# Optimization experiments

Measured on AMD Instinct MI355X. Metric: run time of the kernel, lower is better.

## Reference

```python
import jax, jax.numpy as jnp
import numpy as np

N = 100000   # total nodes across the ragged graph batch
E = 800000   # edges
B = 4096     # graphs
V = 103      # element vocab (embedding rows)
D_IN = 200   # embedding dim
H = 256      # hidden dim


def setup_inputs() -> dict:
    key = jax.random.key(0)
    ks = jax.random.split(key, 20)
    s = 0.05
    return {
        "weight": jax.random.normal(ks[0], (V, D_IN), jnp.float32),
        "sto_x": jax.random.randint(ks[1], (N,), 0, V),
        "sto_edge_index": jax.random.randint(ks[2], (2, E), 0, N),
        "sto_weight": jax.random.uniform(ks[3], (N,), jnp.float32),
        "sto_batch": jnp.sort(jax.random.randint(ks[4], (N,), 0, B)),
        "gW0": jax.random.normal(ks[5], (D_IN, H), jnp.float32) * s,
        "gb0": jnp.zeros((H,), jnp.float32),
        "gW1": jax.random.normal(ks[6], (H, H), jnp.float32) * s,
        "gb1": jnp.zeros((H,), jnp.float32),
        "gW2": jax.random.normal(ks[7], (H, H), jnp.float32) * s,
        "gb2": jnp.zeros((H,), jnp.float32),
        "lstm_Wih": jax.random.normal(ks[8], (4 * H, 2 * H), jnp.float32) * s,
        "lstm_Whh": jax.random.normal(ks[9], (4 * H, H), jnp.float32) * s,
        "lstm_bih": jnp.zeros((4 * H,), jnp.float32),
        "lstm_bhh": jnp.zeros((4 * H,), jnp.float32),
        "mlin_W": jax.random.normal(ks[10], (H, 2 * H), jnp.float32) * s,
        "mlin_b": jnp.zeros((H,), jnp.float32),
        "p0W": jax.random.normal(ks[11], (128, H), jnp.float32) * s,
        "p0b": jnp.zeros((128,), jnp.float32),
        "p1W": jax.random.normal(ks[12], (128, 128), jnp.float32) * s,
        "p1b": jnp.zeros((128,), jnp.float32),
        "p2W": jax.random.normal(ks[13], (1, 128), jnp.float32) * s,
        "p2b": jnp.zeros((1,), jnp.float32),
    }


def reference(weight, sto_x, sto_edge_index, sto_weight, sto_batch,
              gW0, gb0, gW1, gb1, gW2, gb2,
              lstm_Wih, lstm_Whh, lstm_bih, lstm_bhh,
              mlin_W, mlin_b, p0W, p0b, p1W, p1b, p2W, p2b):
    # embedding gather (sto_x - 1, with -1 wrapping to the last row as in torch)
    x = weight[sto_x - 1]

    # --- GCN (3 layers, symmetric norm with self-loops, ReLU between layers) ---
    loop = jnp.arange(N)
    src = jnp.concatenate([sto_edge_index[0], loop])
    dst = jnp.concatenate([sto_edge_index[1], loop])
    deg = jax.ops.segment_sum(jnp.ones_like(dst, jnp.float32), dst, N)
    dinv = jax.lax.rsqrt(jnp.maximum(deg, 1.0))
    norm = (dinv[src] * dinv[dst])[:, None]

    def conv(h_in, W, b):
        hw = h_in @ W                                   # [N, H]
        return jax.ops.segment_sum(hw[src] * norm, dst, N) + b

    x = jax.nn.relu(conv(x, gW0, gb0))
    x = jax.nn.relu(conv(x, gW1, gb1))
    x = conv(x, gW2, gb2)

    # --- stoichiometric weighting + graph-wise scatter sum ---
    wx = x * sto_weight[:, None]                        # [N, H]
    sto = jax.ops.segment_sum(wx, sto_batch, B)         # [B, H]

    # --- Set2Set pooling (2 processing steps, 1-layer LSTM) ---
    h = jnp.zeros((B, H), wx.dtype)
    c = jnp.zeros((B, H), wx.dtype)
    q_star = jnp.zeros((B, 2 * H), wx.dtype)
    for _ in range(2):
        gates = q_star @ lstm_Wih.T + lstm_bih + h @ lstm_Whh.T + lstm_bhh
        i, f, g, o = jnp.split(gates, 4, axis=-1)
        c = jax.nn.sigmoid(f) * c + jax.nn.sigmoid(i) * jnp.tanh(g)
        h = jax.nn.sigmoid(o) * jnp.tanh(c)
        e = jnp.sum(wx * h[sto_batch], axis=-1)         # [N]
        emax = jax.ops.segment_max(e, sto_batch, B)
        a = jnp.exp(e - emax[sto_batch])
        a = a / (jax.ops.segment_sum(a, sto_batch, B)[sto_batch] + 1e-16)
        r = jax.ops.segment_sum(wx * a[:, None], sto_batch, B)
        q_star = jnp.concatenate([h, r], axis=-1)

    mean = q_star @ mlin_W.T + mlin_b + sto
    mean = mean / jnp.maximum(jnp.linalg.norm(mean, axis=1, keepdims=True), 1e-12)

    # --- predictor MLP (LeakyReLU slope 0.01) ---
    y = jax.nn.leaky_relu(mean @ p0W.T + p0b)
    y = jax.nn.leaky_relu(y @ p1W.T + p1b)
    return y @ p2W.T + p2b                              # [B, 1]
```

## Files before the change

### kernel.cpp

```cpp
#include <hip/hip_runtime.h>
#include <math.h>

constexpr int Nn  = 100000;
constexpr int Ee  = 800000;
constexpr int Bb  = 4096;
constexpr int Vv  = 103;
constexpr int DIN = 200;
constexpr int Hh  = 256;

constexpr int SCHUNK = 1024;
constexpr int NSCAN  = (Nn + SCHUNK - 1)/SCHUNK;

using short8 = __attribute__((ext_vector_type(8))) short;
using f32x4  = __attribute__((ext_vector_type(4))) float;

__device__ __forceinline__ float sigf(float x){ return 1.f/(1.f+expf(-x)); }

__device__ __forceinline__ unsigned short f2bf(float f){
  unsigned int u = __float_as_uint(f);
  u += 0x7FFFu + ((u >> 16) & 1u);
  return (unsigned short)(u >> 16);
}
__device__ __forceinline__ float bf2f(unsigned int u){
  return __uint_as_float((u & 0xFFFFu) << 16);
}

constexpr int PW_A = DIN*Hh;
constexpr int PW_B = Hh*Hh;
constexpr int PW_C = Hh*Hh;
constexpr int PW_D = 4*Hh*3*Hh;
constexpr int PW_E = Hh*2*Hh;
constexpr int PW_F = 128*Hh;
constexpr int PW_G = 128*128;
constexpr int PW_H = Bb + 1;
constexpr int PW_I = 4*Hh;
constexpr int PW_TOT = PW_A+PW_B+PW_C+PW_D+PW_E+PW_F+PW_G+PW_H+PW_I;

__global__ void k_prep(const float* __restrict__ gW0, float* __restrict__ gW0t,
                       const float* __restrict__ gW1, unsigned short* __restrict__ gW1tb,
                       const float* __restrict__ gW2, unsigned short* __restrict__ gW2tb,
                       const float* __restrict__ Wih, const float* __restrict__ Whh,
                       unsigned short* __restrict__ Wpb,
                       const float* __restrict__ mW, unsigned short* __restrict__ mWb,
                       const float* __restrict__ p0W, unsigned short* __restrict__ p0Wb,
                       const float* __restrict__ p1W, unsigned short* __restrict__ p1Wb,
                       const int* __restrict__ batch, int* __restrict__ boffs,
                       const float* __restrict__ bih, const float* __restrict__ bhh,
                       float* __restrict__ bsum){
  int idx = blockIdx.x*256 + threadIdx.x;
  if (idx >= PW_TOT) return;
  if (idx < PW_A){
    int r = idx / Hh, c = idx % Hh;
    gW0t[(size_t)c*DIN + r] = gW0[idx];
    return;
  }
  idx -= PW_A;
  if (idx < PW_B){
    int r = idx >> 8, c = idx & 255;
    gW1tb[(size_t)c*Hh + r] = f2bf(gW1[idx]);
    return;
  }
  idx -= PW_B;
  if (idx < PW_C){
    int r = idx >> 8, c = idx & 255;
    gW2tb[(size_t)c*Hh + r] = f2bf(gW2[idx]);
    return;
  }
  idx -= PW_C;
  if (idx < PW_D){
    int g = idx / (3*Hh), j = idx % (3*Hh);
    float v = (j < 2*Hh) ? Wih[(size_t)g*2*Hh + j] : Whh[(size_t)g*Hh + (j - 2*Hh)];
    Wpb[idx] = f2bf(v);
    return;
  }
  idx -= PW_D;
  if (idx < PW_E){ mWb[idx] = f2bf(mW[idx]); return; }
  idx -= PW_E;
  if (idx < PW_F){ p0Wb[idx] = f2bf(p0W[idx]); return; }
  idx -= PW_F;
  if (idx < PW_G){ p1Wb[idx] = f2bf(p1W[idx]); return; }
  idx -= PW_G;
  if (idx < PW_H){
    int b = idx;
    int lo = 0, hi = Nn;
    while (lo < hi){ int mid = (lo+hi)>>1; if (batch[mid] < b) lo = mid+1; else hi = mid; }
    boffs[b] = lo;
    return;
  }
  idx -= PW_H;
  bsum[idx] = bih[idx] + bhh[idx];
}

__global__ void k_count(const int* __restrict__ dst, int* __restrict__ counts){
  int e = blockIdx.x*256 + threadIdx.x;
  if (e < Ee) atomicAdd(&counts[dst[e]], 1);
}

__global__ void k_scan1(const int* __restrict__ counts, int* __restrict__ partial,
                        float* __restrict__ dinv){
  __shared__ int red[256];
  int t = threadIdx.x;
  int base = blockIdx.x*SCHUNK + t*4;
  int s = 0;
  if (base + 3 < Nn){
    int4 v = *reinterpret_cast<const int4*>(counts + base);
    s = v.x+v.y+v.z+v.w;
    dinv[base]   = rsqrtf((float)(v.x + 1));
    dinv[base+1] = rsqrtf((float)(v.y + 1));
    dinv[base+2] = rsqrtf((float)(v.z + 1));
    dinv[base+3] = rsqrtf((float)(v.w + 1));
  } else {
    for (int i=0;i<4;++i) if (base+i<Nn){ int c = counts[base+i]; s += c; dinv[base+i] = rsqrtf((float)(c+1)); }
  }
  red[t] = s; __syncthreads();
  for (int st=128; st>0; st>>=1){ if (t<st) red[t]+=red[t+st]; __syncthreads(); }
  if (t==0) partial[blockIdx.x] = red[0];
}

__global__ void k_scan2(int* __restrict__ partial, int n){
  __shared__ int buf[128];
  int t = threadIdx.x;
  int v = (t < n) ? partial[t] : 0;
  buf[t] = v; __syncthreads();
  for (int off=1; off<128; off<<=1){
    int tv = (t>=off) ? buf[t-off] : 0;
    __syncthreads();
    buf[t] += tv;
    __syncthreads();
  }
  if (t < n) partial[t] = buf[t] - v;
}

__global__ void k_scan3(const int* __restrict__ counts, const int* __restrict__ partial,
                        int* __restrict__ offs, int* __restrict__ fptr){
  __shared__ int red[256];
  int t = threadIdx.x;
  int base = blockIdx.x*SCHUNK + t*4;
  int c0=0,c1=0,c2=0,c3=0;
  if (base + 3 < Nn){ int4 v = *reinterpret_cast<const int4*>(counts + base); c0=v.x;c1=v.y;c2=v.z;c3=v.w; }
  else { if (base<Nn) c0=counts[base]; if (base+1<Nn) c1=counts[base+1];
         if (base+2<Nn) c2=counts[base+2]; if (base+3<Nn) c3=counts[base+3]; }
  int s = c0+c1+c2+c3;
  red[t] = s; __syncthreads();
  for (int off=1; off<256; off<<=1){
    int tv = (t>=off) ? red[t-off] : 0;
    __syncthreads();
    red[t] += tv;
    __syncthreads();
  }
  int run = partial[blockIdx.x] + red[t] - s;
  if (base   < Nn){ offs[base]   = run; fptr[base]   = run; } run += c0;
  if (base+1 < Nn){ offs[base+1] = run; fptr[base+1] = run; } run += c1;
  if (base+2 < Nn){ offs[base+2] = run; fptr[base+2] = run; } run += c2;
  if (base+3 < Nn){ offs[base+3] = run; fptr[base+3] = run; } run += c3;
  if (blockIdx.x == gridDim.x-1 && t == 255) offs[Nn] = partial[blockIdx.x] + red[255];
}

__global__ void k_fill(const int* __restrict__ ei, const float* __restrict__ dinv,
                       const int* __restrict__ sto_x, int* __restrict__ fptr,
                       uint2* __restrict__ epack, unsigned char* __restrict__ evoc){
  int e = blockIdx.x*256 + threadIdx.x;
  if (e >= Ee) return;
  int s = ei[e], d = ei[Ee + e];
  int pos = atomicAdd(&fptr[d], 1);
  epack[pos] = make_uint2((unsigned int)s, __float_as_uint(dinv[s]*dinv[d]));
  int v = sto_x[s];
  evoc[pos] = (unsigned char)((v == 0) ? (Vv-1) : v-1);
}

__global__ void k_conv0(const unsigned short* __restrict__ WG0b, const int* __restrict__ sto_x,
                        const int* __restrict__ offs, const uint2* __restrict__ epack,
                        const unsigned char* __restrict__ evoc, const float* __restrict__ dinv,
                        const float* __restrict__ bias, unsigned short* __restrict__ Xb){
  int wid = threadIdx.x >> 6, lane = threadIdx.x & 63;
  int n = blockIdx.x*4 + wid;
  const uint2* Wv = (const uint2*)WG0b;
  int v0 = sto_x[n]; int r0 = (v0 == 0) ? (Vv-1) : v0-1;
  float dn = dinv[n]; float s2 = dn*dn;
  uint2 w0 = Wv[(size_t)r0*64 + lane];
  float a0 = bf2f(w0.x)*s2, a1 = bf2f(w0.x>>16)*s2;
  float a2 = bf2f(w0.y)*s2, a3 = bf2f(w0.y>>16)*s2;
  int s = offs[n], e = offs[n+1];
  int k = s;
  for (; k + 7 < e; k += 8){
    uint2 ev[8]; int rv[8]; uint2 g[8];
    #pragma unroll
    for (int j = 0; j < 8; ++j){ ev[j] = epack[k+j]; rv[j] = evoc[k+j]; }
    #pragma unroll
    for (int j = 0; j < 8; ++j) g[j] = Wv[(size_t)rv[j]*64 + lane];
    #pragma unroll
    for (int j = 0; j < 8; ++j){
      float nn = __uint_as_float(ev[j].y);
      a0 += bf2f(g[j].x)*nn; a1 += bf2f(g[j].x>>16)*nn;
      a2 += bf2f(g[j].y)*nn; a3 += bf2f(g[j].y>>16)*nn;
    }
  }
  for (; k < e; ++k){
    uint2 ev = epack[k];
    uint2 g = Wv[(size_t)evoc[k]*64 + lane];
    float nn = __uint_as_float(ev.y);
    a0 += bf2f(g.x)*nn; a1 += bf2f(g.x>>16)*nn;
    a2 += bf2f(g.y)*nn; a3 += bf2f(g.y>>16)*nn;
  }
  float4 bv = ((const float4*)bias)[lane];
  a0 = fmaxf(a0 + bv.x, 0.f); a1 = fmaxf(a1 + bv.y, 0.f);
  a2 = fmaxf(a2 + bv.z, 0.f); a3 = fmaxf(a3 + bv.w, 0.f);
  uint2 o;
  o.x = (unsigned int)f2bf(a0) | ((unsigned int)f2bf(a1) << 16);
  o.y = (unsigned int)f2bf(a2) | ((unsigned int)f2bf(a3) << 16);
  ((uint2*)Xb)[(size_t)n*64 + lane] = o;
}

__global__ void k_agg(const unsigned short* __restrict__ Xb, const int* __restrict__ offs,
                      const uint2* __restrict__ epack, const float* __restrict__ dinv,
                      unsigned short* __restrict__ T){
  int wid = threadIdx.x >> 6, lane = threadIdx.x & 63;
  int n = blockIdx.x*4 + wid;
  const uint2* Xv = (const uint2*)Xb;
  uint2 v = Xv[(size_t)n*64 + lane];
  float dn = dinv[n]; float s2 = dn*dn;
  float a0 = bf2f(v.x)*s2, a1 = bf2f(v.x>>16)*s2;
  float a2 = bf2f(v.y)*s2, a3 = bf2f(v.y>>16)*s2;
  int s = offs[n], e = offs[n+1];
  int k = s;
  for (; k + 7 < e; k += 8){
    uint2 ev[8], g[8];
    #pragma unroll
    for (int j = 0; j < 8; ++j) ev[j] = epack[k+j];
    #pragma unroll
    for (int j = 0; j < 8; ++j) g[j] = Xv[(size_t)ev[j].x*64 + lane];
    #pragma unroll
    for (int j = 0; j < 8; ++j){
      float nn = __uint_as_float(ev[j].y);
      a0 += bf2f(g[j].x)*nn; a1 += bf2f(g[j].x>>16)*nn;
      a2 += bf2f(g[j].y)*nn; a3 += bf2f(g[j].y>>16)*nn;
    }
  }
  for (; k + 1 < e; k += 2){
    uint2 e0 = epack[k], e1 = epack[k+1];
    uint2 g0 = Xv[(size_t)e0.x*64 + lane];
    uint2 g1 = Xv[(size_t)e1.x*64 + lane];
    float n0 = __uint_as_float(e0.y), n1 = __uint_as_float(e1.y);
    a0 += bf2f(g0.x)*n0; a1 += bf2f(g0.x>>16)*n0; a2 += bf2f(g0.y)*n0; a3 += bf2f(g0.y>>16)*n0;
    a0 += bf2f(g1.x)*n1; a1 += bf2f(g1.x>>16)*n1; a2 += bf2f(g1.y)*n1; a3 += bf2f(g1.y>>16)*n1;
  }
  if (k < e){
    uint2 e0 = epack[k];
    uint2 g0 = Xv[(size_t)e0.x*64 + lane];
    float n0 = __uint_as_float(e0.y);
    a0 += bf2f(g0.x)*n0; a1 += bf2f(g0.x>>16)*n0;
    a2 += bf2f(g0.y)*n0; a3 += bf2f(g0.y>>16)*n0;
  }
  uint2 o;
  o.x = (unsigned int)f2bf(a0) | ((unsigned int)f2bf(a1) << 16);
  o.y = (unsigned int)f2bf(a2) | ((unsigned int)f2bf(a3) << 16);
  ((uint2*)T)[(size_t)n*64 + lane] = o;
}

__global__ __launch_bounds__(512) void k_gemm64(
    const unsigned short* __restrict__ A, int lda,
    const unsigned short* __restrict__ Bt,
    const float* __restrict__ bias, const float* __restrict__ rowscale,
    const float* __restrict__ addf,
    float* __restrict__ Cf, unsigned short* __restrict__ Cb,
    int M, int K, int Nc, int relu)
{
  __shared__ unsigned short lds[23040];
  unsigned short (*Al)[72] = (unsigned short(*)[72])lds;
  unsigned short (*Bl)[72] = (unsigned short(*)[72])(lds + 64*72);

  int tid = threadIdx.x;
  int w = tid >> 6, lane = tid & 63;
  int wr = (w >> 2)*32, wc = (w & 3)*64;
  int l16 = lane & 15, kh = lane >> 4;
  int rbase = blockIdx.y*64, cbase = blockIdx.x*256;
  int sr = tid >> 3, sb = tid & 7;

  f32x4 acc[2][4] = {};

  for (int k0 = 0; k0 < K; k0 += 64){
    int kk = k0 + sb*8;
    uint4 a0 = make_uint4(0,0,0,0);
    int ar = rbase + sr;
    if (ar < M) a0 = *reinterpret_cast<const uint4*>(A + (size_t)ar*lda + kk);
    uint4 b0 = *reinterpret_cast<const uint4*>(Bt + (size_t)(cbase + sr      )*K + kk);
    uint4 b1 = *reinterpret_cast<const uint4*>(Bt + (size_t)(cbase + sr +  64)*K + kk);
    uint4 b2 = *reinterpret_cast<const uint4*>(Bt + (size_t)(cbase + sr + 128)*K + kk);
    uint4 b3 = *reinterpret_cast<const uint4*>(Bt + (size_t)(cbase + sr + 192)*K + kk);
    __syncthreads();
    *reinterpret_cast<uint4*>(&Al[sr][sb*8])     = a0;
    *reinterpret_cast<uint4*>(&Bl[sr][sb*8])     = b0;
    *reinterpret_cast<uint4*>(&Bl[sr+64][sb*8])  = b1;
    *reinterpret_cast<uint4*>(&Bl[sr+128][sb*8]) = b2;
    *reinterpret_cast<uint4*>(&Bl[sr+192][sb*8]) = b3;
    __syncthreads();

    #pragma unroll
    for (int kq = 0; kq < 2; ++kq){
      short8 af[2], bfv[4];
      #pragma unroll
      for (int m = 0; m < 2; ++m)
        af[m] = *reinterpret_cast<const short8*>(&Al[wr + m*16 + l16][kq*32 + kh*8]);
      #pragma unroll
      for (int n2 = 0; n2 < 4; ++n2)
        bfv[n2] = *reinterpret_cast<const short8*>(&Bl[wc + n2*16 + l16][kq*32 + kh*8]);
      #pragma unroll
      for (int m = 0; m < 2; ++m)
        #pragma unroll
        for (int n2 = 0; n2 < 4; ++n2)
          acc[m][n2] = __builtin_amdgcn_mfma_f32_16x16x32_bf16(af[m], bfv[n2], acc[m][n2], 0, 0, 0);
    }
  }

  if (Cf){
    #pragma unroll
    for (int n2 = 0; n2 < 4; ++n2){
      int col = cbase + wc + n2*16 + l16;
      float bv = bias ? bias[col] : 0.f;
      #pragma unroll
      for (int m = 0; m < 2; ++m){
        #pragma unroll
        for (int i = 0; i < 4; ++i){
          int row = rbase + wr + m*16 + kh*4 + i;
          if (row >= M) continue;
          float v = acc[m][n2][i] + bv;
          if (addf) v += addf[(size_t)row*Nc + col];
          if (rowscale) v *= rowscale[row];
          if (relu == 1) v = fmaxf(v, 0.f);
          else if (relu == 2) v = (v > 0.f) ? v : 0.01f*v;
          Cf[(size_t)row*Nc + col] = v;
        }
      }
    }
  }
  if (Cb){
    __syncthreads();
    unsigned short* eps = lds + w*(32*72);
    #pragma unroll
    for (int n2 = 0; n2 < 4; ++n2){
      int colg = cbase + wc + n2*16 + l16;
      float bv = bias ? bias[colg] : 0.f;
      #pragma unroll
      for (int m = 0; m < 2; ++m){
        #pragma unroll
        for (int i = 0; i < 4; ++i){
          int lrow = m*16 + kh*4 + i;
          int rowg = rbase + wr + lrow;
          float v = acc[m][n2][i] + bv;
          float rs = (rowscale && rowg < M) ? rowscale[rowg] : 1.f;
          v *= rs;
          if (relu == 1) v = fmaxf(v, 0.f);
          else if (relu == 2) v = (v > 0.f) ? v : 0.01f*v;
          eps[lrow*72 + n2*16 + l16] = f2bf(v);
        }
      }
    }
    int c8 = lane & 7;
    #pragma unroll
    for (int rd = 0; rd < 4; ++rd){
      int lrow = rd*8 + (lane >> 3);
      int rowg = rbase + wr + lrow;
      short8 vv = *reinterpret_cast<const short8*>(&eps[lrow*72 + c8*8]);
      if (rowg < M)
        *reinterpret_cast<short8*>(Cb + (size_t)rowg*Nc + cbase + wc + c8*8) = vv;
    }
  }
}

__global__ __launch_bounds__(512) void k_gemm8(
    const unsigned short* __restrict__ A, int lda,
    const unsigned short* __restrict__ Bt,
    const float* __restrict__ bias, const float* __restrict__ rowscale,
    const float* __restrict__ addf,
    float* __restrict__ Cf, unsigned short* __restrict__ Cb,
    int M, int K, int Nc, int relu)
{
  __shared__ unsigned short lds[18432];
  unsigned short (*Al)[40] = (unsigned short(*)[40])lds;
  unsigned short (*Bl)[40] = (unsigned short(*)[40])(lds + 128*40);

  int tid = threadIdx.x;
  int w = tid >> 6, lane = tid & 63;
  int wr = (w >> 1)*32, wc = (w & 1)*64;
  int l16 = lane & 15, kh = lane >> 4;
  int rbase = blockIdx.y*128, cbase = blockIdx.x*128;
  int sr = tid >> 2, sb = tid & 3;

  f32x4 acc[2][4] = {};

  for (int k0 = 0; k0 < K; k0 += 32){
    int kk = k0 + sb*8;
    uint4 a0 = make_uint4(0,0,0,0);
    int ar0 = rbase + sr;
    if (ar0 < M) a0 = *reinterpret_cast<const uint4*>(A + (size_t)ar0*lda + kk);
    uint4 b0 = *reinterpret_cast<const uint4*>(Bt + (size_t)(cbase + sr)*K + kk);
    __syncthreads();
    *reinterpret_cast<uint4*>(&Al[sr][sb*8]) = a0;
    *reinterpret_cast<uint4*>(&Bl[sr][sb*8]) = b0;
    __syncthreads();

    short8 af[2], bfv[4];
    #pragma unroll
    for (int m = 0; m < 2; ++m) af[m] = *reinterpret_cast<const short8*>(&Al[wr + m*16 + l16][kh*8]);
    #pragma unroll
    for (int n2 = 0; n2 < 4; ++n2) bfv[n2] = *reinterpret_cast<const short8*>(&Bl[wc + n2*16 + l16][kh*8]);
    #pragma unroll
    for (int m = 0; m < 2; ++m)
      #pragma unroll
      for (int n2 = 0; n2 < 4; ++n2)
        acc[m][n2] = __builtin_amdgcn_mfma_f32_16x16x32_bf16(af[m], bfv[n2], acc[m][n2], 0, 0, 0);
  }

  if (Cf){
    #pragma unroll
    for (int n2 = 0; n2 < 4; ++n2){
      int col = cbase + wc + n2*16 + l16;
      float bv = bias ? bias[col] : 0.f;
      #pragma unroll
      for (int m = 0; m < 2; ++m){
        #pragma unroll
        for (int i = 0; i < 4; ++i){
          int row = rbase + wr + m*16 + kh*4 + i;
          if (row >= M) continue;
          float v = acc[m][n2][i] + bv;
          if (addf) v += addf[(size_t)row*Nc + col];
          if (rowscale) v *= rowscale[row];
          if (relu == 1) v = fmaxf(v, 0.f);
          else if (relu == 2) v = (v > 0.f) ? v : 0.01f*v;
          Cf[(size_t)row*Nc + col] = v;
        }
      }
    }
  }
  if (Cb){
    __syncthreads();
    unsigned short* eps = lds + w*(32*72);
    #pragma unroll
    for (int n2 = 0; n2 < 4; ++n2){
      int colg = cbase + wc + n2*16 + l16;
      float bv = bias ? bias[colg] : 0.f;
      #pragma unroll
      for (int m = 0; m < 2; ++m){
        #pragma unroll
        for (int i = 0; i < 4; ++i){
          int lrow = m*16 + kh*4 + i;
          int rowg = rbase + wr + lrow;
          float v = acc[m][n2][i] + bv;
          float rs = (rowscale && rowg < M) ? rowscale[rowg] : 1.f;
          v *= rs;
          if (relu == 1) v = fmaxf(v, 0.f);
          else if (relu == 2) v = (v > 0.f) ? v : 0.01f*v;
          eps[lrow*72 + n2*16 + l16] = f2bf(v);
        }
      }
    }
    int c8 = lane & 7;
    #pragma unroll
    for (int rd = 0; rd < 4; ++rd){
      int lrow = rd*8 + (lane >> 3);
      int rowg = rbase + wr + lrow;
      short8 vv = *reinterpret_cast<const short8*>(&eps[lrow*72 + c8*8]);
      if (rowg < M)
        *reinterpret_cast<short8*>(Cb + (size_t)rowg*Nc + cbase + wc + c8*8) = vv;
    }
  }
}

__global__ __launch_bounds__(256) void k_gemm_nt(
    const float* __restrict__ A, const float* __restrict__ Bt,
    float* __restrict__ C, unsigned short* __restrict__ Cb,
    int M, int K, int Nc)
{
  __shared__ float As[64][20];
  __shared__ float Bs[64][20];
  int tid = threadIdx.x;
  int rbase = blockIdx.y*64, cbase = blockIdx.x*64;
  int ty = tid>>4, tx = tid&15;
  int lr = tid>>2, lq = tid&3;
  float acc[4][4] = {};
  for (int k0 = 0; k0 < K; k0 += 16){
    float4 av = make_float4(0,0,0,0), bv = make_float4(0,0,0,0);
    int kk = k0 + lq*4;
    int ar = rbase + lr;
    if (ar < M && kk < K){
      if (kk + 3 < K) av = *reinterpret_cast<const float4*>(A + (size_t)ar*K + kk);
      else { float t0[4] = {0,0,0,0}; for (int i=0; i<4 && kk+i<K; ++i) t0[i] = A[(size_t)ar*K + kk + i];
             av = make_float4(t0[0],t0[1],t0[2],t0[3]); }
    }
    int br = cbase + lr;
    if (br < Nc && kk < K){
      if (kk + 3 < K) bv = *reinterpret_cast<const float4*>(Bt + (size_t)br*K + kk);
      else { float t0[4] = {0,0,0,0}; for (int i=0; i<4 && kk+i<K; ++i) t0[i] = Bt[(size_t)br*K + kk + i];
             bv = make_float4(t0[0],t0[1],t0[2],t0[3]); }
    }
    __syncthreads();
    *reinterpret_cast<float4*>(&As[lr][lq*4]) = av;
    *reinterpret_cast<float4*>(&Bs[lr][lq*4]) = bv;
    __syncthreads();
    #pragma unroll
    for (int kc = 0; kc < 16; kc += 4){
      float4 a4[4], b4[4];
      #pragma unroll
      for (int i=0;i<4;++i) a4[i] = *reinterpret_cast<float4*>(&As[ty*4+i][kc]);
      #pragma unroll
      for (int j=0;j<4;++j) b4[j] = *reinterpret_cast<float4*>(&Bs[tx*4+j][kc]);
      #pragma unroll
      for (int i=0;i<4;++i)
        #pragma unroll
        for (int j=0;j<4;++j)
          acc[i][j] += a4[i].x*b4[j].x + a4[i].y*b4[j].y + a4[i].z*b4[j].z + a4[i].w*b4[j].w;
    }
  }
  #pragma unroll
  for (int i=0;i<4;++i){
    int r = rbase + ty*4 + i;
    if (r >= M) continue;
    #pragma unroll
    for (int j=0;j<4;++j){
      int cc = cbase + tx*4 + j;
      if (cc >= Nc) continue;
      float v = acc[i][j];
      if (C)  C[(size_t)r*Nc + cc] = v;
      if (Cb) Cb[(size_t)r*Nc + cc] = f2bf(v);
    }
  }
}

__global__ void k_lstm(const float* __restrict__ gates, float* __restrict__ cbuf,
                       float* __restrict__ hbuf, unsigned short* __restrict__ qh){
  int idx = blockIdx.x*256 + threadIdx.x;
  if (idx >= Bb*Hh) return;
  int b = idx >> 8, ch = idx & 255;
  const float* g = gates + (size_t)b*4*Hh;
  float ig = sigf(g[ch]);
  float fg = sigf(g[Hh + ch]);
  float gg = tanhf(g[2*Hh + ch]);
  float og = sigf(g[3*Hh + ch]);
  float cn = fg*cbuf[idx] + ig*gg;
  float hn = og*tanhf(cn);
  cbuf[idx] = cn; hbuf[idx] = hn;
  unsigned short hb = f2bf(hn);
  qh[(size_t)b*3*Hh + ch] = hb;
  qh[(size_t)b*3*Hh + 2*Hh + ch] = hb;
}

__global__ void k_pool(const unsigned short* __restrict__ wxb,
                       const float* __restrict__ hbuf,
                       const int* __restrict__ boffs,
                       unsigned short* __restrict__ qh,
                       float* __restrict__ sto, int do_sto){
  int wid = threadIdx.x >> 6, lane = threadIdx.x & 63;
  int g = blockIdx.x*4 + wid;
  if (g >= Bb) return;
  const uint2* Xv = (const uint2*)wxb;
  float4 hv = ((const float4*)hbuf)[(size_t)g*64 + lane];
  int s = boffs[g], e = boffs[g+1];
  float m = -INFINITY, ssum = 0.f;
  float a0=0.f,a1=0.f,a2=0.f,a3=0.f;
  float t0=0.f,t1=0.f,t2=0.f,t3=0.f;
  for (int n = s; n < e; ++n){
    uint2 v = Xv[(size_t)n*64 + lane];
    float x0=bf2f(v.x), x1=bf2f(v.x>>16), x2=bf2f(v.y), x3=bf2f(v.y>>16);
    if (do_sto){ t0+=x0; t1+=x1; t2+=x2; t3+=x3; }
    float d = x0*hv.x + x1*hv.y + x2*hv.z + x3*hv.w;
    #pragma unroll
    for (int mask=32; mask; mask>>=1) d += __shfl_xor(d, mask, 64);
    if (d > m){
      float sc = expf(m - d);
      ssum = ssum*sc + 1.f;
      a0 = a0*sc + x0; a1 = a1*sc + x1; a2 = a2*sc + x2; a3 = a3*sc + x3;
      m = d;
    } else {
      float p = expf(d - m);
      ssum += p;
      a0 += p*x0; a1 += p*x1; a2 += p*x2; a3 += p*x3;
    }
  }
  float inv = 1.f/(ssum + 1e-16f);
  uint2 o;
  o.x = (unsigned int)f2bf(a0*inv) | ((unsigned int)f2bf(a1*inv) << 16);
  o.y = (unsigned int)f2bf(a2*inv) | ((unsigned int)f2bf(a3*inv) << 16);
  ((uint2*)(qh + (size_t)g*3*Hh + Hh))[lane] = o;
  if (do_sto) ((float4*)sto)[(size_t)g*64 + lane] = make_float4(t0,t1,t2,t3);
}

__global__ void k_norm(float* __restrict__ mean, unsigned short* __restrict__ outb){
  __shared__ float red[256];
  int b = blockIdx.x, tid = threadIdx.x;
  float v = mean[(size_t)b*Hh + tid];
  red[tid] = v*v; __syncthreads();
  for (int st=128; st>0; st>>=1){ if (tid<st) red[tid] += red[tid+st]; __syncthreads(); }
  float nrm = fmaxf(sqrtf(red[0]), 1e-12f);
  float o = v/nrm;
  outb[(size_t)b*Hh + tid] = f2bf(o);
}

__global__ void k_out(const float* __restrict__ y1, const float* __restrict__ p2W,
                      const float* __restrict__ p2b, float* __restrict__ out){
  __shared__ float red[128];
  int b = blockIdx.x, tid = threadIdx.x;
  float v = y1[(size_t)b*128 + tid]*p2W[tid];
  red[tid] = v; __syncthreads();
  for (int st=64; st>0; st>>=1){ if (tid<st) red[tid] += red[tid+st]; __syncthreads(); }
  if (tid == 0) out[b] = red[0] + p2b[0];
}

extern "C" void kernel_launch(void* const* d_in, const int* in_sizes, int n_in,
                              void* d_out, int out_size, void* d_ws, size_t ws_size,
                              hipStream_t stream) {
  const float* weight   = (const float*)d_in[0];
  const int*   sto_x    = (const int*)  d_in[1];
  const int*   ei       = (const int*)  d_in[2];
  const float* sto_w    = (const float*)d_in[3];
  const int*   batch    = (const int*)  d_in[4];
  const float* gW0 = (const float*)d_in[5];   const float* gb0 = (const float*)d_in[6];
  const float* gW1 = (const float*)d_in[7];   const float* gb1 = (const float*)d_in[8];
  const float* gW2 = (const float*)d_in[9];   const float* gb2 = (const float*)d_in[10];
  const float* Wih = (const float*)d_in[11];  const float* Whh = (const float*)d_in[12];
  const float* bih = (const float*)d_in[13];  const float* bhh = (const float*)d_in[14];
  const float* mW  = (const float*)d_in[15];  const float* mb  = (const float*)d_in[16];
  const float* p0W = (const float*)d_in[17];  const float* p0b = (const float*)d_in[18];
  const float* p1W = (const float*)d_in[19];  const float* p1b = (const float*)d_in[20];
  const float* p2W = (const float*)d_in[21];  const float* p2b = (const float*)d_in[22];
  float* out = (float*)d_out;

  char* w = (char*)d_ws;
  auto alloc = [&](size_t bytes)->char*{ char* p = w; w += (bytes + 255) & ~size_t(255); return p; };
  unsigned short* Xb = (unsigned short*)alloc((size_t)Nn*Hh*2);
  unsigned short* Tb = (unsigned short*)alloc((size_t)Nn*Hh*2);
  float* WG0   = (float*)alloc((size_t)Vv*Hh*4);
  unsigned short* WG0b = (unsigned short*)alloc((size_t)Vv*Hh*2);
  float* gW0t  = (float*)alloc((size_t)Hh*DIN*4);
  unsigned short* gW1tb = (unsigned short*)alloc((size_t)Hh*Hh*2);
  unsigned short* gW2tb = (unsigned short*)alloc((size_t)Hh*Hh*2);
  unsigned short* Wpb   = (unsigned short*)alloc((size_t)4*Hh*3*Hh*2);
  unsigned short* mWb   = (unsigned short*)alloc((size_t)Hh*2*Hh*2);
  unsigned short* p0Wb  = (unsigned short*)alloc((size_t)128*Hh*2);
  unsigned short* p1Wb  = (unsigned short*)alloc((size_t)128*128*2);
  int*   counts= (int*)  alloc((size_t)Nn*4);
  int*   offs  = (int*)  alloc((size_t)(Nn+1)*4);
  int*   fptr  = (int*)  alloc((size_t)Nn*4);
  int*   spart = (int*)  alloc((size_t)NSCAN*4);
  float* dinv  = (float*)alloc((size_t)Nn*4);
  uint2* epack = (uint2*)alloc((size_t)Ee*8);
  unsigned char* evoc = (unsigned char*)alloc((size_t)Ee);
  int*   boffs = (int*)  alloc((size_t)(Bb+1)*4);
  float* sto   = (float*)alloc((size_t)Bb*Hh*4);
  float* hbuf  = (float*)alloc((size_t)Bb*Hh*4);
  float* cbuf  = (float*)alloc((size_t)Bb*Hh*4);
  unsigned short* qh = (unsigned short*)alloc((size_t)Bb*3*Hh*2);
  float* gates = (float*)alloc((size_t)Bb*4*Hh*4);
  float* bsum  = (float*)alloc((size_t)4*Hh*4);
  float* meanb = (float*)alloc((size_t)Bb*Hh*4);
  unsigned short* meanbb = (unsigned short*)alloc((size_t)Bb*Hh*2);
  unsigned short* y0b = (unsigned short*)alloc((size_t)Bb*128*2);
  float* y1    = (float*)alloc((size_t)Bb*128*4);

  auto gemm8 = [&](const unsigned short* A, int lda, const unsigned short* Bt,
                   const float* bias, const float* rowscale, const float* addf,
                   float* Cf, unsigned short* Cb, int M, int K, int Nc, int relu){
    dim3 g(Nc/128, (M+127)/128);
    k_gemm8<<<g, 512, 0, stream>>>(A, lda, Bt, bias, rowscale, addf, Cf, Cb, M, K, Nc, relu);
  };
  auto gemm64 = [&](const unsigned short* A, int lda, const unsigned short* Bt,
                    const float* bias, const float* rowscale, const float* addf,
                    float* Cf, unsigned short* Cb, int M, int K, int Nc, int relu){
    dim3 g(Nc/256, (M+63)/64);
    k_gemm64<<<g, 512, 0, stream>>>(A, lda, Bt, bias, rowscale, addf, Cf, Cb, M, K, Nc, relu);
  };

  hipMemsetAsync(counts, 0, (size_t)Nn*4, stream);
  hipMemsetAsync(cbuf,  0, (size_t)Bb*Hh*4, stream);
  hipMemsetAsync(qh,    0, (size_t)Bb*3*Hh*2, stream);

  k_prep<<<(PW_TOT+255)/256, 256, 0, stream>>>(
      gW0, gW0t, gW1, gW1tb, gW2, gW2tb, Wih, Whh, Wpb,
      mW, mWb, p0W, p0Wb, p1W, p1Wb, batch, boffs, bih, bhh, bsum);

  k_count<<<(Ee+255)/256, 256, 0, stream>>>(ei + Ee, counts);
  k_scan1<<<NSCAN, 256, 0, stream>>>(counts, spart, dinv);
  k_scan2<<<1, 128, 0, stream>>>(spart, NSCAN);
  k_scan3<<<NSCAN, 256, 0, stream>>>(counts, spart, offs, fptr);
  k_fill<<<(Ee+255)/256, 256, 0, stream>>>(ei, dinv, sto_x, fptr, epack, evoc);

  {
    dim3 g((Hh+63)/64, (Vv+63)/64);
    k_gemm_nt<<<g, 256, 0, stream>>>(weight, gW0t, WG0, WG0b, Vv, DIN, Hh);
  }
  k_conv0<<<Nn/4, 256, 0, stream>>>(WG0b, sto_x, offs, epack, evoc, dinv, gb0, Xb);

  k_agg<<<Nn/4, 256, 0, stream>>>(Xb, offs, epack, dinv, Tb);
  gemm64(Tb, Hh, gW1tb, gb1, nullptr, nullptr, nullptr, Xb, Nn, Hh, Hh, 1);
  k_agg<<<Nn/4, 256, 0, stream>>>(Xb, offs, epack, dinv, Tb);
  gemm64(Tb, Hh, gW2tb, gb2, sto_w, nullptr, nullptr, Xb, Nn, Hh, Hh, 0);

  for (int t = 0; t < 2; ++t){
    gemm64(qh, 3*Hh, Wpb, bsum, nullptr, nullptr, gates, nullptr, Bb, 3*Hh, 4*Hh, 0);
    k_lstm<<<(Bb*Hh+255)/256, 256, 0, stream>>>(gates, cbuf, hbuf, qh);
    k_pool<<<Bb/4, 256, 0, stream>>>(Xb, hbuf, boffs, qh, sto, t == 0);
  }

  gemm64(qh, 3*Hh, mWb, mb, nullptr, sto, meanb, nullptr, Bb, 2*Hh, Hh, 0);
  k_norm<<<Bb, Hh, 0, stream>>>(meanb, meanbb);
  gemm8(meanbb, Hh, p0Wb, p0b, nullptr, nullptr, nullptr, y0b, Bb, Hh, 128, 2);
  gemm8(y0b, 128, p1Wb, p1b, nullptr, nullptr, y1, nullptr, Bb, 128, 128, 2);
  k_out<<<Bb, 128, 0, stream>>>(y1, p2W, p2b, out);
}
```

Baseline: 551.0 us.

## Fold constant first Set2Set LSTM step and shrink second-step gate GEMM

Because h, c and q_star start at zero, the first LSTM step gives the same h0/c0 for every graph, so it is computed once by a tiny kernel instead of a full gate GEMM over all graphs. The second step's gate contribution from h0 (Wih's h-part plus Whh) is folded into a per-gate constant bias, leaving a GEMM with K=256 over only the attention readout r. The pool kernel is also unrolled by two nodes to overlap loads and shuffle reductions, and the memsets for the zeroed LSTM state and the unused fp32 embedding output are dropped. In exchange it adds small extra kernels, and it relies on the initial state being zero, which the reference specifies.

```diff
diff --git a/kernel.cpp b/kernel.cpp
--- a/kernel.cpp
+++ b/kernel.cpp
@@ -28,7 +28,7 @@
 constexpr int PW_A = DIN*Hh;
 constexpr int PW_B = Hh*Hh;
 constexpr int PW_C = Hh*Hh;
-constexpr int PW_D = 4*Hh*3*Hh;
+constexpr int PW_D = 4*Hh*Hh;
 constexpr int PW_E = Hh*2*Hh;
 constexpr int PW_F = 128*Hh;
 constexpr int PW_G = 128*128;
@@ -39,8 +39,7 @@
 __global__ void k_prep(const float* __restrict__ gW0, float* __restrict__ gW0t,
                        const float* __restrict__ gW1, unsigned short* __restrict__ gW1tb,
                        const float* __restrict__ gW2, unsigned short* __restrict__ gW2tb,
-                       const float* __restrict__ Wih, const float* __restrict__ Whh,
-                       unsigned short* __restrict__ Wpb,
+                       const float* __restrict__ Wih, unsigned short* __restrict__ WihRb,
                        const float* __restrict__ mW, unsigned short* __restrict__ mWb,
                        const float* __restrict__ p0W, unsigned short* __restrict__ p0Wb,
                        const float* __restrict__ p1W, unsigned short* __restrict__ p1Wb,
@@ -68,9 +67,8 @@
   }
   idx -= PW_C;
   if (idx < PW_D){
-    int g = idx / (3*Hh), j = idx % (3*Hh);
-    float v = (j < 2*Hh) ? Wih[(size_t)g*2*Hh + j] : Whh[(size_t)g*Hh + (j - 2*Hh)];
-    Wpb[idx] = f2bf(v);
+    int gi = idx >> 8, k = idx & 255;
+    WihRb[idx] = f2bf(Wih[(size_t)gi*2*Hh + Hh + k]);
     return;
   }
   idx -= PW_D;
@@ -89,6 +87,30 @@
   }
   idx -= PW_H;
   bsum[idx] = bih[idx] + bhh[idx];
+}
+
+__global__ void k_h0(const float* __restrict__ bsum, float* __restrict__ h0,
+                     float* __restrict__ c0){
+  int ch = threadIdx.x;
+  float ig = sigf(bsum[ch]);
+  float gg = tanhf(bsum[2*Hh + ch]);
+  float og = sigf(bsum[3*Hh + ch]);
+  float cn = ig*gg;
+  float hn = og*tanhf(cn);
+  c0[ch] = cn; h0[ch] = hn;
+}
+
+__global__ void k_gconst(const float* __restrict__ Wih, const float* __restrict__ Whh,
+                         const float* __restrict__ bsum, const float* __restrict__ h0,
+                         float* __restrict__ gconst){
+  int wid = threadIdx.x >> 6, lane = threadIdx.x & 63;
+  int gi = blockIdx.x*4 + wid;
+  float4 hv = ((const float4*)h0)[lane];
+  float4 a = *reinterpret_cast<const float4*>(Wih + (size_t)gi*2*Hh + lane*4);
+  float4 b = *reinterpret_cast<const float4*>(Whh + (size_t)gi*Hh  + lane*4);
+  float ssum = hv.x*(a.x+b.x) + hv.y*(a.y+b.y) + hv.z*(a.z+b.z) + hv.w*(a.w+b.w);
+  for (int off=32; off; off>>=1) ssum += __shfl_down(ssum, off, 64);
+  if (lane == 0) gconst[gi] = bsum[gi] + ssum;
 }
 
 __global__ void k_count(const int* __restrict__ dst, int* __restrict__ counts){
@@ -468,8 +490,7 @@
 
 __global__ __launch_bounds__(256) void k_gemm_nt(
     const float* __restrict__ A, const float* __restrict__ Bt,
-    float* __restrict__ C, unsigned short* __restrict__ Cb,
-    int M, int K, int Nc)
+    unsigned short* __restrict__ Cb, int M, int K, int Nc)
 {
   __shared__ float As[64][20];
   __shared__ float Bs[64][20];
@@ -519,15 +540,13 @@
     for (int j=0;j<4;++j){
       int cc = cbase + tx*4 + j;
       if (cc >= Nc) continue;
-      float v = acc[i][j];
-      if (C)  C[(size_t)r*Nc + cc] = v;
-      if (Cb) Cb[(size_t)r*Nc + cc] = f2bf(v);
-    }
-  }
-}
-
-__global__ void k_lstm(const float* __restrict__ gates, float* __restrict__ cbuf,
-                       float* __restrict__ hbuf, unsigned short* __restrict__ qh){
+      Cb[(size_t)r*Nc + cc] = f2bf(acc[i][j]);
+    }
+  }
+}
+
+__global__ void k_lstm1(const float* __restrict__ gates, const float* __restrict__ c0,
+                        float* __restrict__ hbuf, unsigned short* __restrict__ qh2){
   int idx = blockIdx.x*256 + threadIdx.x;
   if (idx >= Bb*Hh) return;
   int b = idx >> 8, ch = idx & 255;
@@ -536,51 +555,82 @@
   float fg = sigf(g[Hh + ch]);
   float gg = tanhf(g[2*Hh + ch]);
   float og = sigf(g[3*Hh + ch]);
-  float cn = fg*cbuf[idx] + ig*gg;
+  float cn = fg*c0[ch] + ig*gg;
   float hn = og*tanhf(cn);
-  cbuf[idx] = cn; hbuf[idx] = hn;
-  unsigned short hb = f2bf(hn);
-  qh[(size_t)b*3*Hh + ch] = hb;
-  qh[(size_t)b*3*Hh + 2*Hh + ch] = hb;
+  hbuf[idx] = hn;
+  qh2[(size_t)b*2*Hh + ch] = f2bf(hn);
 }
 
 __global__ void k_pool(const unsigned short* __restrict__ wxb,
-                       const float* __restrict__ hbuf,
+                       const float* __restrict__ hsrc, int hper,
                        const int* __restrict__ boffs,
-                       unsigned short* __restrict__ qh,
+                       unsigned short* __restrict__ rout, int rstride,
                        float* __restrict__ sto, int do_sto){
   int wid = threadIdx.x >> 6, lane = threadIdx.x & 63;
   int g = blockIdx.x*4 + wid;
   if (g >= Bb) return;
   const uint2* Xv = (const uint2*)wxb;
-  float4 hv = ((const float4*)hbuf)[(size_t)g*64 + lane];
+  float4 hv = hper ? ((const float4*)hsrc)[(size_t)g*64 + lane]
+                   : ((const float4*)hsrc)[lane];
   int s = boffs[g], e = boffs[g+1];
   float m = -INFINITY, ssum = 0.f;
   float a0=0.f,a1=0.f,a2=0.f,a3=0.f;
   float t0=0.f,t1=0.f,t2=0.f,t3=0.f;
-  for (int n = s; n < e; ++n){
-    uint2 v = Xv[(size_t)n*64 + lane];
-    float x0=bf2f(v.x), x1=bf2f(v.x>>16), x2=bf2f(v.y), x3=bf2f(v.y>>16);
-    if (do_sto){ t0+=x0; t1+=x1; t2+=x2; t3+=x3; }
-    float d = x0*hv.x + x1*hv.y + x2*hv.z + x3*hv.w;
-    #pragma unroll
-    for (int mask=32; mask; mask>>=1) d += __shfl_xor(d, mask, 64);
-    if (d > m){
-      float sc = expf(m - d);
+  int n = s;
+  for (; n + 1 < e; n += 2){
+    uint2 v0 = Xv[(size_t)n*64 + lane];
+    uint2 v1 = Xv[(size_t)(n+1)*64 + lane];
+    float x00=bf2f(v0.x), x01=bf2f(v0.x>>16), x02=bf2f(v0.y), x03=bf2f(v0.y>>16);
+    float x10=bf2f(v1.x), x11=bf2f(v1.x>>16), x12=bf2f(v1.y), x13=bf2f(v1.y>>16);
+    if (do_sto){ t0+=x00+x10; t1+=x01+x11; t2+=x02+x12; t3+=x03+x13; }
+    float d0 = x00*hv.x + x01*hv.y + x02*hv.z + x03*hv.w;
+    float d1 = x10*hv.x + x11*hv.y + x12*hv.z + x13*hv.w;
+    #pragma unroll
+    for (int mask=32; mask; mask>>=1){
+      d0 += __shfl_xor(d0, mask, 64);
+      d1 += __shfl_xor(d1, mask, 64);
+    }
+    if (d0 > m){
+      float sc = expf(m - d0);
       ssum = ssum*sc + 1.f;
-      a0 = a0*sc + x0; a1 = a1*sc + x1; a2 = a2*sc + x2; a3 = a3*sc + x3;
-      m = d;
+      a0 = a0*sc + x00; a1 = a1*sc + x01; a2 = a2*sc + x02; a3 = a3*sc + x03;
+      m = d0;
     } else {
-      float p = expf(d - m);
-      ssum += p;
-      a0 += p*x0; a1 += p*x1; a2 += p*x2; a3 += p*x3;
+      float p = expf(d0 - m);
+      ssum += p; a0 += p*x00; a1 += p*x01; a2 += p*x02; a3 += p*x03;
+    }
+    if (d1 > m){
+      float sc = expf(m - d1);
+      ssum = ssum*sc + 1.f;
+      a0 = a0*sc + x10; a1 = a1*sc + x11; a2 = a2*sc + x12; a3 = a3*sc + x13;
+      m = d1;
+    } else {
+      float p = expf(d1 - m);
+      ssum += p; a0 += p*x10; a1 += p*x11; a2 += p*x12; a3 += p*x13;
+    }
+  }
+  if (n < e){
+    uint2 v0 = Xv[(size_t)n*64 + lane];
+    float x00=bf2f(v0.x), x01=bf2f(v0.x>>16), x02=bf2f(v0.y), x03=bf2f(v0.y>>16);
+    if (do_sto){ t0+=x00; t1+=x01; t2+=x02; t3+=x03; }
+    float d0 = x00*hv.x + x01*hv.y + x02*hv.z + x03*hv.w;
+    #pragma unroll
+    for (int mask=32; mask; mask>>=1) d0 += __shfl_xor(d0, mask, 64);
+    if (d0 > m){
+      float sc = expf(m - d0);
+      ssum = ssum*sc + 1.f;
+      a0 = a0*sc + x00; a1 = a1*sc + x01; a2 = a2*sc + x02; a3 = a3*sc + x03;
+      m = d0;
+    } else {
+      float p = expf(d0 - m);
+      ssum += p; a0 += p*x00; a1 += p*x01; a2 += p*x02; a3 += p*x03;
     }
   }
   float inv = 1.f/(ssum + 1e-16f);
   uint2 o;
   o.x = (unsigned int)f2bf(a0*inv) | ((unsigned int)f2bf(a1*inv) << 16);
   o.y = (unsigned int)f2bf(a2*inv) | ((unsigned int)f2bf(a3*inv) << 16);
-  ((uint2*)(qh + (size_t)g*3*Hh + Hh))[lane] = o;
+  ((uint2*)(rout + (size_t)g*rstride))[lane] = o;
   if (do_sto) ((float4*)sto)[(size_t)g*64 + lane] = make_float4(t0,t1,t2,t3);
 }
 
@@ -628,12 +678,11 @@
   auto alloc = [&](size_t bytes)->char*{ char* p = w; w += (bytes + 255) & ~size_t(255); return p; };
   unsigned short* Xb = (unsigned short*)alloc((size_t)Nn*Hh*2);
   unsigned short* Tb = (unsigned short*)alloc((size_t)Nn*Hh*2);
-  float* WG0   = (float*)alloc((size_t)Vv*Hh*4);
   unsigned short* WG0b = (unsigned short*)alloc((size_t)Vv*Hh*2);
   float* gW0t  = (float*)alloc((size_t)Hh*DIN*4);
   unsigned short* gW1tb = (unsigned short*)alloc((size_t)Hh*Hh*2);
   unsigned short* gW2tb = (unsigned short*)alloc((size_t)Hh*Hh*2);
-  unsigned short* Wpb   = (unsigned short*)alloc((size_t)4*Hh*3*Hh*2);
+  unsigned short* WihRb = (unsigned short*)alloc((size_t)4*Hh*Hh*2);
   unsigned short* mWb   = (unsigned short*)alloc((size_t)Hh*2*Hh*2);
   unsigned short* p0Wb  = (unsigned short*)alloc((size_t)128*Hh*2);
   unsigned short* p1Wb  = (unsigned short*)alloc((size_t)128*128*2);
@@ -647,10 +696,13 @@
   int*   boffs = (int*)  alloc((size_t)(Bb+1)*4);
   float* sto   = (float*)alloc((size_t)Bb*Hh*4);
   float* hbuf  = (float*)alloc((size_t)Bb*Hh*4);
-  float* cbuf  = (float*)alloc((size_t)Bb*Hh*4);
-  unsigned short* qh = (unsigned short*)alloc((size_t)Bb*3*Hh*2);
+  unsigned short* r0b = (unsigned short*)alloc((size_t)Bb*Hh*2);
+  unsigned short* qh2 = (unsigned short*)alloc((size_t)Bb*2*Hh*2);
   float* gates = (float*)alloc((size_t)Bb*4*Hh*4);
   float* bsum  = (float*)alloc((size_t)4*Hh*4);
+  float* h0    = (float*)alloc((size_t)Hh*4);
+  float* c0    = (float*)alloc((size_t)Hh*4);
+  float* gconst= (float*)alloc((size_t)4*Hh*4);
   float* meanb = (float*)alloc((size_t)Bb*Hh*4);
   unsigned short* meanbb = (unsigned short*)alloc((size_t)Bb*Hh*2);
   unsigned short* y0b = (unsigned short*)alloc((size_t)Bb*128*2);
@@ -670,12 +722,12 @@
   };
 
   hipMemsetAsync(counts, 0, (size_t)Nn*4, stream);
-  hipMemsetAsync(cbuf,  0, (size_t)Bb*Hh*4, stream);
-  hipMemsetAsync(qh,    0, (size_t)Bb*3*Hh*2, stream);
 
   k_prep<<<(PW_TOT+255)/256, 256, 0, stream>>>(
-      gW0, gW0t, gW1, gW1tb, gW2, gW2tb, Wih, Whh, Wpb,
+      gW0, gW0t, gW1, gW1tb, gW2, gW2tb, Wih, WihRb,
       mW, mWb, p0W, p0Wb, p1W, p1Wb, batch, boffs, bih, bhh, bsum);
+  k_h0<<<1, 256, 0, stream>>>(bsum, h0, c0);
+  k_gconst<<<Bb*4*Hh ? (4*Hh)/4 : 1, 256, 0, stream>>>(Wih, Whh, bsum, h0, gconst);
 
   k_count<<<(Ee+255)/256, 256, 0, stream>>>(ei + Ee, counts);
   k_scan1<<<NSCAN, 256, 0, stream>>>(counts, spart, dinv);
@@ -685,7 +737,7 @@
 
   {
     dim3 g((Hh+63)/64, (Vv+63)/64);
-    k_gemm_nt<<<g, 256, 0, stream>>>(weight, gW0t, WG0, WG0b, Vv, DIN, Hh);
+    k_gemm_nt<<<g, 256, 0, stream>>>(weight, gW0t, WG0b, Vv, DIN, Hh);
   }
   k_conv0<<<Nn/4, 256, 0, stream>>>(WG0b, sto_x, offs, epack, evoc, dinv, gb0, Xb);
 
@@ -694,13 +746,12 @@
   k_agg<<<Nn/4, 256, 0, stream>>>(Xb, offs, epack, dinv, Tb);
   gemm64(Tb, Hh, gW2tb, gb2, sto_w, nullptr, nullptr, Xb, Nn, Hh, Hh, 0);
 
-  for (int t = 0; t < 2; ++t){
-    gemm64(qh, 3*Hh, Wpb, bsum, nullptr, nullptr, gates, nullptr, Bb, 3*Hh, 4*Hh, 0);
-    k_lstm<<<(Bb*Hh+255)/256, 256, 0, stream>>>(gates, cbuf, hbuf, qh);
-    k_pool<<<Bb/4, 256, 0, stream>>>(Xb, hbuf, boffs, qh, sto, t == 0);
-  }
-
-  gemm64(qh, 3*Hh, mWb, mb, nullptr, sto, meanb, nullptr, Bb, 2*Hh, Hh, 0);
+  k_pool<<<Bb/4, 256, 0, stream>>>(Xb, h0, 0, boffs, r0b, Hh, sto, 1);
+  gemm64(r0b, Hh, WihRb, gconst, nullptr, nullptr, gates, nullptr, Bb, Hh, 4*Hh, 0);
+  k_lstm1<<<(Bb*Hh+255)/256, 256, 0, stream>>>(gates, c0, hbuf, qh2);
+  k_pool<<<Bb/4, 256, 0, stream>>>(Xb, hbuf, 1, boffs, qh2 + Hh, 2*Hh, nullptr, 0);
+
+  gemm64(qh2, 2*Hh, mWb, mb, nullptr, sto, meanb, nullptr, Bb, 2*Hh, Hh, 0);
   k_norm<<<Bb, Hh, 0, stream>>>(meanb, meanbb);
   gemm8(meanbb, Hh, p0Wb, p0b, nullptr, nullptr, nullptr, y0b, Bb, Hh, 128, 2);
   gemm8(y0b, 128, p1Wb, p1b, nullptr, nullptr, y1, nullptr, Bb, 128, 128, 2);
```

After: 490.4 us. 11.0% less time.
